# Optimization experiments

Measured on AMD Instinct MI355X. Metric: run time of the kernel, lower is better.

## Reference

```python
import jax, jax.numpy as jnp
import numpy as np

K = 3; STRIDE = 1; PAD = 1; DIL = 1; KN = K * K * K  # num_pts = 27


def _trilinear_sample(vol, grid):
    """F.grid_sample 3D, mode=bilinear, padding=zeros, align_corners=False.
    vol: (C, D, H, W); grid: (od, oh, ow, 3) with xyz order in [-1, 1].
    Returns (C, od, oh, ow)."""
    C, D, H, W = vol.shape
    # unnormalize (align_corners=False)
    ix = ((grid[..., 0] + 1.0) * W - 1.0) * 0.5
    iy = ((grid[..., 1] + 1.0) * H - 1.0) * 0.5
    iz = ((grid[..., 2] + 1.0) * D - 1.0) * 0.5
    x0 = jnp.floor(ix); y0 = jnp.floor(iy); z0 = jnp.floor(iz)
    out = jnp.zeros((C,) + grid.shape[:-1], vol.dtype)
    for dz in (0, 1):
        for dy in (0, 1):
            for dx in (0, 1):
                xc = x0 + dx; yc = y0 + dy; zc = z0 + dz
                w = (1.0 - jnp.abs(ix - xc)) * (1.0 - jnp.abs(iy - yc)) * (1.0 - jnp.abs(iz - zc))
                valid = (xc >= 0) & (xc < W) & (yc >= 0) & (yc < H) & (zc >= 0) & (zc < D)
                xi = jnp.clip(xc, 0, W - 1).astype(jnp.int32)
                yi = jnp.clip(yc, 0, H - 1).astype(jnp.int32)
                zi = jnp.clip(zc, 0, D - 1).astype(jnp.int32)
                val = vol[:, zi, yi, xi]  # (C, od, oh, ow)
                out = out + val * (w * valid.astype(vol.dtype))[None]
    return out


def setup_inputs() -> dict:
    key = jax.random.key(0)
    k1, k2, k3 = jax.random.split(key, 3)
    N, C, D, H, W = 2, 64, 16, 32, 32
    inp = jax.random.normal(k1, (N, C, D, H, W), dtype=jnp.float32)
    offset = jax.random.normal(k2, (N, KN * 3, D, H, W), dtype=jnp.float32)
    weight = jax.random.normal(k3, (64, 64, KN), dtype=jnp.float32) * 0.05
    return {"input": inp, "offset": offset, "weight": weight}


def reference(input, offset, weight):
    N, C, D, H, W = input.shape
    od, oh, ow = offset.shape[2], offset.shape[3], offset.shape[4]
    f32 = input.dtype
    # base sampling mesh (align_corners=True style normalization, as original)
    z = (jnp.arange(od) * STRIDE - PAD + ((K - 1) // 2) * DIL).astype(f32)
    y = (jnp.arange(oh) * STRIDE - PAD + ((K - 1) // 2) * DIL).astype(f32)
    x = (jnp.arange(ow) * STRIDE - PAD + ((K - 1) // 2) * DIL).astype(f32)
    mz, my, mx = jnp.meshgrid(z, y, x, indexing="ij")
    norm = lambda v, S: (v - (S - 1) / 2.0) / ((S - 1) / 2.0)
    mesh = jnp.stack([norm(mx, W), norm(my, H), norm(mz, D)], axis=-1)  # (od,oh,ow,3)
    # offsets: channel layout per kernel point is (dz, dy, dx)
    off = offset.reshape(N, KN, 3, od, oh, ow)
    goff = jnp.stack([
        off[:, :, 2] / ((W - 1) / 2.0),
        off[:, :, 1] / ((H - 1) / 2.0),
        off[:, :, 0] / ((D - 1) / 2.0),
    ], axis=-1)  # (N, KN, od, oh, ow, 3) xyz
    grid = mesh[None, None] + goff
    # per-batch, per-kernel-point trilinear gather -> (N, KN, C, od, oh, ow)
    sampled = jax.vmap(lambda v, g: jax.vmap(lambda gg: _trilinear_sample(v, gg))(g))(input, grid)
    # grouped matmul: weight (O, C, KN) flattened C-major matches sampled layout
    out = jnp.einsum("ock,nkcdhw->nodhw", weight, sampled)
    return out
```

## Files before the change

### kernel.cpp

```cpp
#include <hip/hip_runtime.h>

typedef __attribute__((ext_vector_type(8))) short short8;
typedef __attribute__((ext_vector_type(8))) _Float16 half8;
typedef __attribute__((ext_vector_type(4))) float floatx4;

constexpr int NB  = 2;
constexpr int CC  = 64;
constexpr int DD  = 16;
constexpr int HH  = 32;
constexpr int WW  = 32;
constexpr int KN_ = 27;
constexpr int OC  = 64;
constexpr int DHW = DD * HH * WW;

__device__ __forceinline__ unsigned short f2h(float f) {
    _Float16 h = (_Float16)f;
    return *(unsigned short*)&h;
}

__global__ __launch_bounds__(256) void k_prep(const float* __restrict__ in,
                                              const float* __restrict__ w,
                                              unsigned int* __restrict__ outu,
                                              unsigned short* __restrict__ wf) {
    int bid = blockIdx.x;
    int t = threadIdx.x;
    if (bid < 512) {
        __shared__ float tile[64][65];
        int n  = bid >> 8;
        int v0 = (bid & 255) << 6;
        int lane = t & 63, row = t >> 6;
#pragma unroll
        for (int i = 0; i < 16; ++i) {
            int c = (i << 2) + row;
            tile[c][lane] = in[(size_t)(n * CC + c) * DHW + v0 + lane];
        }
        __syncthreads();
#pragma unroll
        for (int i = 0; i < 8; ++i) {
            int flat = i * 256 + t;
            int v = flat >> 5, cd = flat & 31;
            unsigned int lo = f2h(tile[2 * cd][v]);
            unsigned int hi = f2h(tile[2 * cd + 1][v]);
            outu[(size_t)(n * DHW + v0 + v) * 32 + cd] = lo | (hi << 16);
        }
    } else {
        int f = (bid - 512) * 256 + t;
        int i  = f & 7;
        int l  = (f >> 3) & 63;
        int wv = (f >> 9) & 3;
        int cc = (f >> 11) & 1;
        int k  = f >> 12;
        int o = wv * 16 + (l & 15);
        int c = cc * 32 + ((l >> 4) << 3) + i;
        wf[f] = f2h(w[(o * CC + c) * KN_ + k]);
    }
}

__global__ __launch_bounds__(256, 4) void k_main(const unsigned short* __restrict__ inp,
                                                 const unsigned short* __restrict__ wf,
                                                 const float* __restrict__ offs,
                                                 float* __restrict__ out) {
    __shared__ unsigned short S[2 * 32 * 64];

    int t   = threadIdx.x;
    int bid = blockIdx.x;
    int n   = bid >> 9;
    int p0  = (bid & 511) << 5;

    int sp = t >> 3;
    int cg = t & 7;
    int pa = p0 + sp;
    int dpos = pa >> 10, hpos = (pa >> 5) & 31, wpos = pa & 31;

    int wv = t >> 6, l = t & 63;
    int lrow = l & 15, lk = l >> 4;

    floatx4 acc0 = {0.f, 0.f, 0.f, 0.f};
    floatx4 acc1 = {0.f, 0.f, 0.f, 0.f};

    const float* offb = offs + (size_t)n * (3 * KN_) * DHW + pa;
    const unsigned short* inb = inp + ((size_t)n * DHW << 6);

    const int woff = sp * 64 + ((cg ^ (sp & 7)) << 3);
    const int prow1 = 16 + lrow;
    const int roff00 = lrow  * 64 + (((0 + lk) ^ (lrow  & 7)) << 3);
    const int roff10 = lrow  * 64 + (((4 + lk) ^ (lrow  & 7)) << 3);
    const int roff01 = prow1 * 64 + (((0 + lk) ^ (prow1 & 7)) << 3);
    const int roff11 = prow1 * 64 + (((4 + lk) ^ (prow1 & 7)) << 3);

    for (int k = 0; k < KN_; ++k) {
        const half8 wa0 = *(const half8*)(wf + (((k << 3) + 0 + wv) << 9) + (l << 3));
        const half8 wa1 = *(const half8*)(wf + (((k << 3) + 4 + wv) << 9) + (l << 3));

        float oz = offb[(k * 3 + 0) * DHW];
        float oy = offb[(k * 3 + 1) * DHW];
        float ox = offb[(k * 3 + 2) * DHW];
        float ix = ((float)wpos + ox) * (32.0f / 31.0f) - 0.5f;
        float iy = ((float)hpos + oy) * (32.0f / 31.0f) - 0.5f;
        float iz = ((float)dpos + oz) * (16.0f / 15.0f) - 0.5f;
        float xf = floorf(ix), yf = floorf(iy), zf = floorf(iz);
        float fx = ix - xf, fy = iy - yf, fz = iz - zf;
        int x0 = (int)xf, y0 = (int)yf, z0 = (int)zf;

        float wx0 = ((unsigned)x0       < (unsigned)WW) ? 1.f - fx : 0.f;
        float wx1 = ((unsigned)(x0 + 1) < (unsigned)WW) ? fx       : 0.f;
        float wy0 = ((unsigned)y0       < (unsigned)HH) ? 1.f - fy : 0.f;
        float wy1 = ((unsigned)(y0 + 1) < (unsigned)HH) ? fy       : 0.f;
        float wz0 = ((unsigned)z0       < (unsigned)DD) ? 1.f - fz : 0.f;
        float wz1 = ((unsigned)(z0 + 1) < (unsigned)DD) ? fz       : 0.f;

        int xc0 = min(max(x0, 0), WW - 1), xc1 = min(max(x0 + 1, 0), WW - 1);
        int yc0 = min(max(y0, 0), HH - 1), yc1 = min(max(y0 + 1, 0), HH - 1);
        int zc0 = min(max(z0, 0), DD - 1), zc1 = min(max(z0 + 1, 0), DD - 1);

        float wzy00 = wz0 * wy0, wzy01 = wz0 * wy1, wzy10 = wz1 * wy0, wzy11 = wz1 * wy1;
        int b00 = (zc0 * HH + yc0) * WW, b01 = (zc0 * HH + yc1) * WW;
        int b10 = (zc1 * HH + yc0) * WW, b11 = (zc1 * HH + yc1) * WW;

        const int vox[8] = {b00 + xc0, b00 + xc1, b01 + xc0, b01 + xc1,
                            b10 + xc0, b10 + xc1, b11 + xc0, b11 + xc1};
        const float cwt[8] = {wzy00 * wx0, wzy00 * wx1, wzy01 * wx0, wzy01 * wx1,
                              wzy10 * wx0, wzy10 * wx1, wzy11 * wx0, wzy11 * wx1};

        half8 acc = {0, 0, 0, 0, 0, 0, 0, 0};
#pragma unroll
        for (int cr = 0; cr < 8; ++cr) {
            const half8 v = *(const half8*)(inb + ((size_t)vox[cr] << 6) + (cg << 3));
            _Float16 wh = (_Float16)cwt[cr];
            half8 w8 = {wh, wh, wh, wh, wh, wh, wh, wh};
            acc += v * w8;
        }
        *(half8*)(S + ((k & 1) << 11) + woff) = acc;

        __syncthreads();

        const unsigned short* Sb = S + ((k & 1) << 11);
        const half8 bf00 = *(const half8*)(Sb + roff00);
        const half8 bf10 = *(const half8*)(Sb + roff10);
        const half8 bf01 = *(const half8*)(Sb + roff01);
        const half8 bf11 = *(const half8*)(Sb + roff11);
        acc0 = __builtin_amdgcn_mfma_f32_16x16x32_f16(wa0, bf00, acc0, 0, 0, 0);
        acc0 = __builtin_amdgcn_mfma_f32_16x16x32_f16(wa1, bf10, acc0, 0, 0, 0);
        acc1 = __builtin_amdgcn_mfma_f32_16x16x32_f16(wa0, bf01, acc1, 0, 0, 0);
        acc1 = __builtin_amdgcn_mfma_f32_16x16x32_f16(wa1, bf11, acc1, 0, 0, 0);
    }

    float* ob = out + ((size_t)n * OC + (wv << 4) + (lk << 2)) * DHW + p0 + lrow;
#pragma unroll
    for (int r = 0; r < 4; ++r) {
        ob[r * DHW]      = acc0[r];
        ob[r * DHW + 16] = acc1[r];
    }
}

__global__ __launch_bounds__(256) void k_fallback(const float* __restrict__ inp,
                                                  const float* __restrict__ wt,
                                                  const float* __restrict__ offs,
                                                  float* __restrict__ out) {
    __shared__ float Slds[64][68];
    __shared__ float Wlds[64 * 64];
    int bid = blockIdx.x;
    int n = bid >> 8;
    int p0 = (bid & 255) * 64;
    int t = threadIdx.x;
    int cq = t & 15, c0 = cq << 2, pslot = t >> 4;
    int ob = (t & 15) << 2, pb = (t >> 4) << 2;
    int swz_w = (((cq & 7) ^ (cq >> 3)) << 2);
    float acc[4][4] = {};
    const float* offbase = offs + (size_t)n * (KN_ * 3) * DHW;
    for (int k = 0; k < KN_; ++k) {
#pragma unroll
        for (int i = 0; i < 16; ++i) {
            int f = i * 256 + t;
            int o = f & 63, c = f >> 6;
            Wlds[f] = wt[(o * CC + c) * KN_ + k];
        }
#pragma unroll
        for (int j = 0; j < 4; ++j) {
            int pl = pslot + 16 * j;
            int pa = p0 + pl;
            int d = pa >> 10, h = (pa >> 5) & 31, w = pa & 31;
            float offz = offbase[(k * 3 + 0) * DHW + pa];
            float offy = offbase[(k * 3 + 1) * DHW + pa];
            float offx = offbase[(k * 3 + 2) * DHW + pa];
            float ix = ((float)w + offx) * (32.0f / 31.0f) - 0.5f;
            float iy = ((float)h + offy) * (32.0f / 31.0f) - 0.5f;
            float iz = ((float)d + offz) * (16.0f / 15.0f) - 0.5f;
            float xf = floorf(ix), yf = floorf(iy), zf = floorf(iz);
            float fx = ix - xf, fy = iy - yf, fz = iz - zf;
            int x0 = (int)xf, y0 = (int)yf, z0 = (int)zf;
            float wx0 = 1.0f - fx, wx1 = fx, wy0 = 1.0f - fy, wy1 = fy, wz0 = 1.0f - fz, wz1 = fz;
            float s0 = 0.f, s1 = 0.f, s2 = 0.f, s3 = 0.f;
#pragma unroll
            for (int dz = 0; dz < 2; ++dz) {
                int zc = z0 + dz;
                if ((unsigned)zc >= (unsigned)DD) continue;
                float wz = dz ? wz1 : wz0;
#pragma unroll
                for (int dy = 0; dy < 2; ++dy) {
                    int yc = y0 + dy;
                    if ((unsigned)yc >= (unsigned)HH) continue;
                    float wzy = wz * (dy ? wy1 : wy0);
#pragma unroll
                    for (int dx = 0; dx < 2; ++dx) {
                        int xc = x0 + dx;
                        if ((unsigned)xc >= (unsigned)WW) continue;
                        float wf = wzy * (dx ? wx1 : wx0);
                        int vox = (zc * HH + yc) * WW + xc;
                        const float* b = inp + (size_t)(n * CC + c0) * DHW + vox;
                        s0 += wf * b[0]; s1 += wf * b[DHW];
                        s2 += wf * b[2 * DHW]; s3 += wf * b[3 * DHW];
                    }
                }
            }
            int plw = pl ^ swz_w;
            Slds[c0 + 0][plw] = s0; Slds[c0 + 1][plw] = s1;
            Slds[c0 + 2][plw] = s2; Slds[c0 + 3][plw] = s3;
        }
        __syncthreads();
#pragma unroll
        for (int c = 0; c < 64; ++c) {
            const int g = ((c >> 2) & 7) ^ (c >> 5);
            float4 wv = *(const float4*)(Wlds + c * 64 + ob);
            float4 sv = *(const float4*)(&Slds[c][pb ^ (g << 2)]);
            float wa[4] = {wv.x, wv.y, wv.z, wv.w};
            float sa[4] = {sv.x, sv.y, sv.z, sv.w};
#pragma unroll
            for (int i = 0; i < 4; ++i)
#pragma unroll
                for (int jj = 0; jj < 4; ++jj) acc[i][jj] += wa[i] * sa[jj];
        }
        __syncthreads();
    }
#pragma unroll
    for (int i = 0; i < 4; ++i) {
        float4 vv;
        vv.x = acc[i][0]; vv.y = acc[i][1]; vv.z = acc[i][2]; vv.w = acc[i][3];
        *(float4*)(out + (size_t)(n * OC + ob + i) * DHW + p0 + pb) = vv;
    }
}

extern "C" void kernel_launch(void* const* d_in, const int* in_sizes, int n_in,
                              void* d_out, int out_size, void* d_ws, size_t ws_size,
                              hipStream_t stream) {
    const float* inp = (const float*)d_in[0];
    const float* off = (const float*)d_in[1];
    const float* wgt = (const float*)d_in[2];
    float* out = (float*)d_out;

    const size_t in_f16_bytes = (size_t)NB * DHW * CC * 2;
    const size_t wf_bytes     = (size_t)KN_ * 2 * 4 * 64 * 8 * 2;
    if (ws_size >= in_f16_bytes + wf_bytes) {
        unsigned int*   in_t = (unsigned int*)d_ws;
        unsigned short* w_f  = (unsigned short*)((char*)d_ws + in_f16_bytes);
        k_prep<<<dim3(512 + 432), dim3(256), 0, stream>>>(inp, wgt, in_t, w_f);
        k_main<<<dim3(NB * 512), dim3(256), 0, stream>>>((const unsigned short*)in_t, w_f, off, out);
    } else {
        k_fallback<<<dim3(NB * 256), dim3(256), 0, stream>>>(inp, wgt, off, out);
    }
}
```

Before: 119.9 us.

## Split kernel-point loop across two block halves with separate reduction kernel

Splits the 27 kernel-point loop into two halves (0..13, 14..26) handled by separate blocks. Each half writes a partial output to workspace, and a new elementwise kernel sums the two. This doubles the block count to raise occupancy and parallelism, and launch bounds are raised to 8 waves. It also software-prefetches the next kernel point's offsets. The cost is an extra launch plus about 16 MB of partial-buffer traffic.

```diff
diff --git a/kernel.cpp b/kernel.cpp
--- a/kernel.cpp
+++ b/kernel.cpp
@@ -10,8 +10,10 @@
 constexpr int HH  = 32;
 constexpr int WW  = 32;
 constexpr int KN_ = 27;
+constexpr int KSP = 14;
 constexpr int OC  = 64;
 constexpr int DHW = DD * HH * WW;
+constexpr size_t OUT_ELEMS = (size_t)NB * OC * DHW;
 
 __device__ __forceinline__ unsigned short f2h(float f) {
     _Float16 h = (_Float16)f;
@@ -56,16 +58,21 @@
     }
 }
 
-__global__ __launch_bounds__(256, 4) void k_main(const unsigned short* __restrict__ inp,
+template <int MODE>
+__global__ __launch_bounds__(256, 8) void k_main(const unsigned short* __restrict__ inp,
                                                  const unsigned short* __restrict__ wf,
                                                  const float* __restrict__ offs,
-                                                 float* __restrict__ out) {
+                                                 float* __restrict__ dst) {
     __shared__ unsigned short S[2 * 32 * 64];
 
     int t   = threadIdx.x;
     int bid = blockIdx.x;
-    int n   = bid >> 9;
-    int p0  = (bid & 511) << 5;
+    int half = MODE ? (bid >> 10) : 0;
+    int n    = (bid >> 9) & 1;
+    int p0   = (bid & 511) << 5;
+    int k0   = half ? KSP : 0;
+    int k1   = MODE ? (half ? KN_ : KSP) : KN_;
+    float* base = dst + (size_t)half * OUT_ELEMS;
 
     int sp = t >> 3;
     int cg = t & 7;
@@ -88,13 +95,21 @@
     const int roff01 = prow1 * 64 + (((0 + lk) ^ (prow1 & 7)) << 3);
     const int roff11 = prow1 * 64 + (((4 + lk) ^ (prow1 & 7)) << 3);
 
-    for (int k = 0; k < KN_; ++k) {
+    float oz = offb[(k0 * 3 + 0) * DHW];
+    float oy = offb[(k0 * 3 + 1) * DHW];
+    float ox = offb[(k0 * 3 + 2) * DHW];
+
+    for (int k = k0; k < k1; ++k) {
+        float noz = 0.f, noy = 0.f, nox = 0.f;
+        if (k + 1 < k1) {
+            noz = offb[((k + 1) * 3 + 0) * DHW];
+            noy = offb[((k + 1) * 3 + 1) * DHW];
+            nox = offb[((k + 1) * 3 + 2) * DHW];
+        }
+
         const half8 wa0 = *(const half8*)(wf + (((k << 3) + 0 + wv) << 9) + (l << 3));
         const half8 wa1 = *(const half8*)(wf + (((k << 3) + 4 + wv) << 9) + (l << 3));
 
-        float oz = offb[(k * 3 + 0) * DHW];
-        float oy = offb[(k * 3 + 1) * DHW];
-        float ox = offb[(k * 3 + 2) * DHW];
         float ix = ((float)wpos + ox) * (32.0f / 31.0f) - 0.5f;
         float iy = ((float)hpos + oy) * (32.0f / 31.0f) - 0.5f;
         float iz = ((float)dpos + oz) * (16.0f / 15.0f) - 0.5f;
@@ -131,6 +146,8 @@
             acc += v * w8;
         }
         *(half8*)(S + ((k & 1) << 11) + woff) = acc;
+
+        oz = noz; oy = noy; ox = nox;
 
         __syncthreads();
 
@@ -145,12 +162,23 @@
         acc1 = __builtin_amdgcn_mfma_f32_16x16x32_f16(wa1, bf11, acc1, 0, 0, 0);
     }
 
-    float* ob = out + ((size_t)n * OC + (wv << 4) + (lk << 2)) * DHW + p0 + lrow;
+    float* ob = base + ((size_t)n * OC + (wv << 4) + (lk << 2)) * DHW + p0 + lrow;
 #pragma unroll
     for (int r = 0; r < 4; ++r) {
         ob[r * DHW]      = acc0[r];
         ob[r * DHW + 16] = acc1[r];
     }
+}
+
+__global__ __launch_bounds__(256) void k_red(const float4* __restrict__ a,
+                                             const float4* __restrict__ b,
+                                             float4* __restrict__ o) {
+    int i = blockIdx.x * 256 + threadIdx.x;
+    float4 va = a[i], vb = b[i];
+    float4 vo;
+    vo.x = va.x + vb.x; vo.y = va.y + vb.y;
+    vo.z = va.z + vb.z; vo.w = va.w + vb.w;
+    o[i] = vo;
 }
 
 __global__ __launch_bounds__(256) void k_fallback(const float* __restrict__ inp,
@@ -250,11 +278,24 @@
 
     const size_t in_f16_bytes = (size_t)NB * DHW * CC * 2;
     const size_t wf_bytes     = (size_t)KN_ * 2 * 4 * 64 * 8 * 2;
-    if (ws_size >= in_f16_bytes + wf_bytes) {
+    const size_t part_bytes   = OUT_ELEMS * sizeof(float);
+    const size_t need_small   = in_f16_bytes + wf_bytes;
+    const size_t need_big     = need_small + 2 * part_bytes;
+
+    if (ws_size >= need_small) {
         unsigned int*   in_t = (unsigned int*)d_ws;
         unsigned short* w_f  = (unsigned short*)((char*)d_ws + in_f16_bytes);
         k_prep<<<dim3(512 + 432), dim3(256), 0, stream>>>(inp, wgt, in_t, w_f);
-        k_main<<<dim3(NB * 512), dim3(256), 0, stream>>>((const unsigned short*)in_t, w_f, off, out);
+        if (ws_size >= need_big) {
+            float* part = (float*)((char*)d_ws + need_small);
+            k_main<1><<<dim3(NB * 512 * 2), dim3(256), 0, stream>>>(
+                (const unsigned short*)in_t, w_f, off, part);
+            k_red<<<dim3((int)(OUT_ELEMS / 4 / 256)), dim3(256), 0, stream>>>(
+                (const float4*)part, (const float4*)(part + OUT_ELEMS), (float4*)out);
+        } else {
+            k_main<0><<<dim3(NB * 512), dim3(256), 0, stream>>>(
+                (const unsigned short*)in_t, w_f, off, out);
+        }
     } else {
         k_fallback<<<dim3(NB * 256), dim3(256), 0, stream>>>(inp, wgt, off, out);
     }
```

Result: slower. 122.4 us (+2.1%).

## Precompute sampling records per chunk in LDS and shrink tiles to 16 points

Applied to the files above, without the earlier changes.

The main kernel now uses 128-thread blocks covering 16 output points each, with each wave computing 32 output channels, and twice as many blocks. Offset loading and trilinear coordinate/weight math is hoisted into a cooperative per-chunk phase (9 kernel points at a time). That phase packs voxel indices and fp16 corner weights into LDS records, so the gather loop only reads them back. The block index mapping interleaves the two batches. The aim is to remove redundant per-thread coordinate math (previously repeated across the 8 channel-group threads) and raise occupancy, at the cost of extra LDS, barriers, and fp16-rounded corner weights.

```diff
diff --git a/kernel.cpp b/kernel.cpp
--- a/kernel.cpp
+++ b/kernel.cpp
@@ -1,6 +1,5 @@
 #include <hip/hip_runtime.h>
 
-typedef __attribute__((ext_vector_type(8))) short short8;
 typedef __attribute__((ext_vector_type(8))) _Float16 half8;
 typedef __attribute__((ext_vector_type(4))) float floatx4;
 
@@ -12,6 +11,8 @@
 constexpr int KN_ = 27;
 constexpr int OC  = 64;
 constexpr int DHW = DD * HH * WW;
+constexpr int TP  = 16;
+constexpr int KCH = 9;
 
 __device__ __forceinline__ unsigned short f2h(float f) {
     _Float16 h = (_Float16)f;
@@ -47,109 +48,139 @@
         int f = (bid - 512) * 256 + t;
         int i  = f & 7;
         int l  = (f >> 3) & 63;
-        int wv = (f >> 9) & 3;
+        int ot = (f >> 9) & 3;
         int cc = (f >> 11) & 1;
         int k  = f >> 12;
-        int o = wv * 16 + (l & 15);
+        int o = ot * 16 + (l & 15);
         int c = cc * 32 + ((l >> 4) << 3) + i;
         wf[f] = f2h(w[(o * CC + c) * KN_ + k]);
     }
 }
 
-__global__ __launch_bounds__(256, 4) void k_main(const unsigned short* __restrict__ inp,
+__global__ __launch_bounds__(128, 6) void k_main(const unsigned short* __restrict__ inp,
                                                  const unsigned short* __restrict__ wf,
                                                  const float* __restrict__ offs,
                                                  float* __restrict__ out) {
-    __shared__ unsigned short S[2 * 32 * 64];
+    __shared__ unsigned short S[2 * TP * 64];
+    __shared__ unsigned int   SU[KCH * TP * 12];
 
     int t   = threadIdx.x;
     int bid = blockIdx.x;
-    int n   = bid >> 9;
-    int p0  = (bid & 511) << 5;
+    int n   = (bid >> 2) & 1;
+    int idx = ((bid >> 3) << 2) | (bid & 3);
+    int p0  = idx << 4;
 
     int sp = t >> 3;
     int cg = t & 7;
-    int pa = p0 + sp;
-    int dpos = pa >> 10, hpos = (pa >> 5) & 31, wpos = pa & 31;
-
     int wv = t >> 6, l = t & 63;
     int lrow = l & 15, lk = l >> 4;
 
+    const float* offb = offs + (size_t)n * (3 * KN_) * DHW + p0;
+    const char*  inb  = (const char*)(inp + ((size_t)n * DHW << 6));
+
     floatx4 acc0 = {0.f, 0.f, 0.f, 0.f};
     floatx4 acc1 = {0.f, 0.f, 0.f, 0.f};
 
-    const float* offb = offs + (size_t)n * (3 * KN_) * DHW + pa;
-    const unsigned short* inb = inp + ((size_t)n * DHW << 6);
-
-    const int woff = sp * 64 + ((cg ^ (sp & 7)) << 3);
-    const int prow1 = 16 + lrow;
-    const int roff00 = lrow  * 64 + (((0 + lk) ^ (lrow  & 7)) << 3);
-    const int roff10 = lrow  * 64 + (((4 + lk) ^ (lrow  & 7)) << 3);
-    const int roff01 = prow1 * 64 + (((0 + lk) ^ (prow1 & 7)) << 3);
-    const int roff11 = prow1 * 64 + (((4 + lk) ^ (prow1 & 7)) << 3);
-
-    for (int k = 0; k < KN_; ++k) {
-        const half8 wa0 = *(const half8*)(wf + (((k << 3) + 0 + wv) << 9) + (l << 3));
-        const half8 wa1 = *(const half8*)(wf + (((k << 3) + 4 + wv) << 9) + (l << 3));
-
-        float oz = offb[(k * 3 + 0) * DHW];
-        float oy = offb[(k * 3 + 1) * DHW];
-        float ox = offb[(k * 3 + 2) * DHW];
-        float ix = ((float)wpos + ox) * (32.0f / 31.0f) - 0.5f;
-        float iy = ((float)hpos + oy) * (32.0f / 31.0f) - 0.5f;
-        float iz = ((float)dpos + oz) * (16.0f / 15.0f) - 0.5f;
-        float xf = floorf(ix), yf = floorf(iy), zf = floorf(iz);
-        float fx = ix - xf, fy = iy - yf, fz = iz - zf;
-        int x0 = (int)xf, y0 = (int)yf, z0 = (int)zf;
-
-        float wx0 = ((unsigned)x0       < (unsigned)WW) ? 1.f - fx : 0.f;
-        float wx1 = ((unsigned)(x0 + 1) < (unsigned)WW) ? fx       : 0.f;
-        float wy0 = ((unsigned)y0       < (unsigned)HH) ? 1.f - fy : 0.f;
-        float wy1 = ((unsigned)(y0 + 1) < (unsigned)HH) ? fy       : 0.f;
-        float wz0 = ((unsigned)z0       < (unsigned)DD) ? 1.f - fz : 0.f;
-        float wz1 = ((unsigned)(z0 + 1) < (unsigned)DD) ? fz       : 0.f;
-
-        int xc0 = min(max(x0, 0), WW - 1), xc1 = min(max(x0 + 1, 0), WW - 1);
-        int yc0 = min(max(y0, 0), HH - 1), yc1 = min(max(y0 + 1, 0), HH - 1);
-        int zc0 = min(max(z0, 0), DD - 1), zc1 = min(max(z0 + 1, 0), DD - 1);
-
-        float wzy00 = wz0 * wy0, wzy01 = wz0 * wy1, wzy10 = wz1 * wy0, wzy11 = wz1 * wy1;
-        int b00 = (zc0 * HH + yc0) * WW, b01 = (zc0 * HH + yc1) * WW;
-        int b10 = (zc1 * HH + yc0) * WW, b11 = (zc1 * HH + yc1) * WW;
-
-        const int vox[8] = {b00 + xc0, b00 + xc1, b01 + xc0, b01 + xc1,
-                            b10 + xc0, b10 + xc1, b11 + xc0, b11 + xc1};
-        const float cwt[8] = {wzy00 * wx0, wzy00 * wx1, wzy01 * wx0, wzy01 * wx1,
-                              wzy10 * wx0, wzy10 * wx1, wzy11 * wx0, wzy11 * wx1};
-
-        half8 acc = {0, 0, 0, 0, 0, 0, 0, 0};
-#pragma unroll
-        for (int cr = 0; cr < 8; ++cr) {
-            const half8 v = *(const half8*)(inb + ((size_t)vox[cr] << 6) + (cg << 3));
-            _Float16 wh = (_Float16)cwt[cr];
-            half8 w8 = {wh, wh, wh, wh, wh, wh, wh, wh};
-            acc += v * w8;
-        }
-        *(half8*)(S + ((k & 1) << 11) + woff) = acc;
-
-        __syncthreads();
-
-        const unsigned short* Sb = S + ((k & 1) << 11);
-        const half8 bf00 = *(const half8*)(Sb + roff00);
-        const half8 bf10 = *(const half8*)(Sb + roff10);
-        const half8 bf01 = *(const half8*)(Sb + roff01);
-        const half8 bf11 = *(const half8*)(Sb + roff11);
-        acc0 = __builtin_amdgcn_mfma_f32_16x16x32_f16(wa0, bf00, acc0, 0, 0, 0);
-        acc0 = __builtin_amdgcn_mfma_f32_16x16x32_f16(wa1, bf10, acc0, 0, 0, 0);
-        acc1 = __builtin_amdgcn_mfma_f32_16x16x32_f16(wa0, bf01, acc1, 0, 0, 0);
-        acc1 = __builtin_amdgcn_mfma_f32_16x16x32_f16(wa1, bf11, acc1, 0, 0, 0);
-    }
-
-    float* ob = out + ((size_t)n * OC + (wv << 4) + (lk << 2)) * DHW + p0 + lrow;
+    const int cgo   = cg << 4;
+    const int woff  = sp * 64 + ((cg ^ (sp & 7)) << 3);
+    const int roff0 = lrow * 64 + (((0 | lk) ^ (lrow & 7)) << 3);
+    const int roff1 = lrow * 64 + (((4 | lk) ^ (lrow & 7)) << 3);
+
+    for (int ch = 0; ch < 3; ++ch) {
+        __syncthreads();
+
+        for (int si = t; si < KCH * TP; si += 128) {
+            int kk = si >> 4, p = si & 15;
+            int k  = ch * KCH + kk;
+            int pa = p0 + p;
+            int dpos = pa >> 10, hpos = (pa >> 5) & 31, wpos = pa & 31;
+
+            float oz = offb[(k * 3 + 0) * DHW + p];
+            float oy = offb[(k * 3 + 1) * DHW + p];
+            float ox = offb[(k * 3 + 2) * DHW + p];
+            float ix = ((float)wpos + ox) * (32.0f / 31.0f) - 0.5f;
+            float iy = ((float)hpos + oy) * (32.0f / 31.0f) - 0.5f;
+            float iz = ((float)dpos + oz) * (16.0f / 15.0f) - 0.5f;
+            float xf = floorf(ix), yf = floorf(iy), zf = floorf(iz);
+            float fx = ix - xf, fy = iy - yf, fz = iz - zf;
+            int x0 = (int)xf, y0 = (int)yf, z0 = (int)zf;
+
+            float wx0 = ((unsigned)x0       < (unsigned)WW) ? 1.f - fx : 0.f;
+            float wx1 = ((unsigned)(x0 + 1) < (unsigned)WW) ? fx       : 0.f;
+            float wy0 = ((unsigned)y0       < (unsigned)HH) ? 1.f - fy : 0.f;
+            float wy1 = ((unsigned)(y0 + 1) < (unsigned)HH) ? fy       : 0.f;
+            float wz0 = ((unsigned)z0       < (unsigned)DD) ? 1.f - fz : 0.f;
+            float wz1 = ((unsigned)(z0 + 1) < (unsigned)DD) ? fz       : 0.f;
+
+            int xc0 = min(max(x0, 0), WW - 1), xc1 = min(max(x0 + 1, 0), WW - 1);
+            int yc0 = min(max(y0, 0), HH - 1), yc1 = min(max(y0 + 1, 0), HH - 1);
+            int zc0 = min(max(z0, 0), DD - 1), zc1 = min(max(z0 + 1, 0), DD - 1);
+
+            float wzy00 = wz0 * wy0, wzy01 = wz0 * wy1, wzy10 = wz1 * wy0, wzy11 = wz1 * wy1;
+            unsigned int b00 = (zc0 * HH + yc0) * WW, b01 = (zc0 * HH + yc1) * WW;
+            unsigned int b10 = (zc1 * HH + yc0) * WW, b11 = (zc1 * HH + yc1) * WW;
+
+            uint4 vp, wp;
+            vp.x = (b00 + xc0) | ((b00 + xc1) << 16);
+            vp.y = (b01 + xc0) | ((b01 + xc1) << 16);
+            vp.z = (b10 + xc0) | ((b10 + xc1) << 16);
+            vp.w = (b11 + xc0) | ((b11 + xc1) << 16);
+            wp.x = (unsigned int)f2h(wzy00 * wx0) | ((unsigned int)f2h(wzy00 * wx1) << 16);
+            wp.y = (unsigned int)f2h(wzy01 * wx0) | ((unsigned int)f2h(wzy01 * wx1) << 16);
+            wp.z = (unsigned int)f2h(wzy10 * wx0) | ((unsigned int)f2h(wzy10 * wx1) << 16);
+            wp.w = (unsigned int)f2h(wzy11 * wx0) | ((unsigned int)f2h(wzy11 * wx1) << 16);
+
+            unsigned int* rec = SU + si * 12;
+            *(uint4*)rec       = vp;
+            *(uint4*)(rec + 4) = wp;
+        }
+        __syncthreads();
+
+        for (int kk = 0; kk < KCH; ++kk) {
+            int k = ch * KCH + kk;
+
+            const half8 wa00 = *(const half8*)(wf + ((((k << 1) | 0) * 4 + (wv << 1) + 0) << 9) + (l << 3));
+            const half8 wa01 = *(const half8*)(wf + ((((k << 1) | 1) * 4 + (wv << 1) + 0) << 9) + (l << 3));
+            const half8 wa10 = *(const half8*)(wf + ((((k << 1) | 0) * 4 + (wv << 1) + 1) << 9) + (l << 3));
+            const half8 wa11 = *(const half8*)(wf + ((((k << 1) | 1) * 4 + (wv << 1) + 1) << 9) + (l << 3));
+
+            const unsigned int* rec = SU + (kk * TP + sp) * 12;
+            const uint4 vp = *(const uint4*)rec;
+            const uint4 wp = *(const uint4*)(rec + 4);
+            const unsigned int vpa[4] = {vp.x, vp.y, vp.z, vp.w};
+            const unsigned int wpa[4] = {wp.x, wp.y, wp.z, wp.w};
+
+            half8 accv = {0, 0, 0, 0, 0, 0, 0, 0};
+#pragma unroll
+            for (int cr = 0; cr < 8; ++cr) {
+                unsigned int vd = vpa[cr >> 1];
+                unsigned int wd = wpa[cr >> 1];
+                unsigned int voxb = ((cr & 1) ? (vd >> 16) : (vd & 0xffffu)) << 7;
+                unsigned short wu = (cr & 1) ? (unsigned short)(wd >> 16) : (unsigned short)wd;
+                _Float16 wh = *(_Float16*)&wu;
+                const half8 v = *(const half8*)(inb + voxb + cgo);
+                half8 w8 = {wh, wh, wh, wh, wh, wh, wh, wh};
+                accv += v * w8;
+            }
+            *(half8*)(S + ((k & 1) << 10) + woff) = accv;
+
+            __syncthreads();
+
+            const unsigned short* Sb = S + ((k & 1) << 10);
+            const half8 bf0 = *(const half8*)(Sb + roff0);
+            const half8 bf1 = *(const half8*)(Sb + roff1);
+            acc0 = __builtin_amdgcn_mfma_f32_16x16x32_f16(wa00, bf0, acc0, 0, 0, 0);
+            acc0 = __builtin_amdgcn_mfma_f32_16x16x32_f16(wa01, bf1, acc0, 0, 0, 0);
+            acc1 = __builtin_amdgcn_mfma_f32_16x16x32_f16(wa10, bf0, acc1, 0, 0, 0);
+            acc1 = __builtin_amdgcn_mfma_f32_16x16x32_f16(wa11, bf1, acc1, 0, 0, 0);
+        }
+    }
+
+    float* ob = out + ((size_t)n * OC + (wv << 5) + (lk << 2)) * DHW + p0 + lrow;
 #pragma unroll
     for (int r = 0; r < 4; ++r) {
-        ob[r * DHW]      = acc0[r];
-        ob[r * DHW + 16] = acc1[r];
+        ob[r * DHW]              = acc0[r];
+        ob[r * DHW + (DHW << 4)] = acc1[r];
     }
 }
 
@@ -250,11 +281,13 @@
 
     const size_t in_f16_bytes = (size_t)NB * DHW * CC * 2;
     const size_t wf_bytes     = (size_t)KN_ * 2 * 4 * 64 * 8 * 2;
+
     if (ws_size >= in_f16_bytes + wf_bytes) {
         unsigned int*   in_t = (unsigned int*)d_ws;
         unsigned short* w_f  = (unsigned short*)((char*)d_ws + in_f16_bytes);
         k_prep<<<dim3(512 + 432), dim3(256), 0, stream>>>(inp, wgt, in_t, w_f);
-        k_main<<<dim3(NB * 512), dim3(256), 0, stream>>>((const unsigned short*)in_t, w_f, off, out);
+        k_main<<<dim3(NB * 1024), dim3(128), 0, stream>>>(
+            (const unsigned short*)in_t, w_f, off, out);
     } else {
         k_fallback<<<dim3(NB * 256), dim3(256), 0, stream>>>(inp, wgt, off, out);
     }
```

After: 113.9 us. 5.0% less time.
